# Performance work log

Hardware: AMD Instinct MI355X
Metric: run time of the kernel (lower is better)

The kernel has to match this reference:

```python
import jax, jax.numpy as jnp
import numpy as np

NUM_HEADS = 16
EPS = 1e-6  # torch LayerNorm default is 1e-5; module uses nn.LayerNorm default
LN_EPS = 1e-5


def layer_norm(x, w, b, eps=LN_EPS):
    # normalize over last dim (head_dim), matching infer_layer_norm
    mu = jnp.mean(x, axis=-1, keepdims=True)
    xc = x - mu
    var = jnp.mean(xc * xc, axis=-1, keepdims=True)
    return xc / jnp.sqrt(var + eps) * w + b


def setup_inputs() -> dict:
    key = jax.random.key(0)
    ks = jax.random.split(key, 4)
    B, N, C = 2, 4096, 1024
    H = NUM_HEADS
    D = C // H
    x = jax.random.normal(ks[0], (B, N, C), dtype=jnp.float32)
    qkv_w = jax.random.normal(ks[1], (3 * C, C), dtype=jnp.float32) * (C ** -0.5)
    qkv_b = jax.random.normal(ks[2], (3 * C,), dtype=jnp.float32) * 0.02
    q_norm_w = jnp.ones((D,), dtype=jnp.float32)
    q_norm_b = jnp.zeros((D,), dtype=jnp.float32)
    k_norm_w = jnp.ones((D,), dtype=jnp.float32)
    k_norm_b = jnp.zeros((D,), dtype=jnp.float32)
    proj_w = jax.random.normal(ks[3], (C, C), dtype=jnp.float32) * (C ** -0.5)
    proj_b = jnp.zeros((C,), dtype=jnp.float32)
    return {"x": x, "qkv_w": qkv_w, "qkv_b": qkv_b,
            "q_norm_w": q_norm_w, "q_norm_b": q_norm_b,
            "k_norm_w": k_norm_w, "k_norm_b": k_norm_b,
            "proj_w": proj_w, "proj_b": proj_b}


def reference(x, qkv_w, qkv_b, q_norm_w, q_norm_b, k_norm_w, k_norm_b, proj_w, proj_b):
    B, N, C = x.shape
    H = NUM_HEADS
    D = C // H
    scale = D ** -0.5
    # QKV projection: torch Linear uses y = x @ W^T + b
    qkv = x @ qkv_w.T + qkv_b                      # [B,N,3C]
    qkv = qkv.reshape(B, N, 3, H, D).transpose(2, 0, 3, 1, 4)  # [3,B,H,N,D]
    q, k, v = qkv[0], qkv[1], qkv[2]
    # per-head qk layernorm
    q = layer_norm(q, q_norm_w, q_norm_b)
    k = layer_norm(k, k_norm_w, k_norm_b)
    # scaled dot product attention
    attn = jnp.einsum('bhqd,bhkd->bhqk', q * scale, k)
    attn = jax.nn.softmax(attn, axis=-1)
    out = jnp.einsum('bhqk,bhkd->bhqd', attn, v)   # [B,H,N,D]
    out = out.transpose(0, 2, 1, 3).reshape(B, N, C)
    return out @ proj_w.T + proj_b
```

## Files before the change

kernel.cpp:

```cpp
#include <hip/hip_runtime.h>
#include <hip/hip_bf16.h>

#define NB 2
#define NN 4096
#define NC 1024
#define NH 16
#define ND 64
#define NM (NB*NN)
#define NK 1024
#define J_QKV 3072
#define QSCALE 0.18033688011112042f

typedef unsigned short u16;
typedef unsigned int   u32;
typedef __attribute__((ext_vector_type(8)))  __bf16 bf16x8;
typedef __attribute__((ext_vector_type(4)))  float  f32x4;
typedef __attribute__((ext_vector_type(16))) float  f32x16;

__device__ __forceinline__ u16 f2bf(float f) {
    unsigned int i = __builtin_bit_cast(unsigned int, f);
    unsigned int lsb = (i >> 16) & 1u;
    i += 0x7fffu + lsb;
    return (u16)(i >> 16);
}
__device__ __forceinline__ float fast_exp2(float x) {
#if __has_builtin(__builtin_amdgcn_exp2f)
    return __builtin_amdgcn_exp2f(x);
#else
    return exp2f(x);
#endif
}
__device__ __forceinline__ u32 pkbf(float a, float b) {
    u32 r;
    asm("v_cvt_pk_bf16_f32 %0, %1, %2" : "=v"(r) : "v"(a), "v"(b));
    return r;
}
typedef struct { u32 x, y; } u32pair;
__device__ __forceinline__ u32pair swap32(u32 a, u32 b) {
#if __has_builtin(__builtin_amdgcn_permlane32_swap)
    auto r = __builtin_amdgcn_permlane32_swap((int)a, (int)b, false, false);
    u32pair o; o.x = (u32)r[0]; o.y = (u32)r[1]; return o;
#else
    const bool hi = (threadIdx.x & 32) != 0;
    u32 as = (u32)__shfl_xor((int)a, 32);
    u32 bs = (u32)__shfl_xor((int)b, 32);
    u32pair o; o.x = hi ? bs : a; o.y = hi ? b : as; return o;
#endif
}

__device__ __forceinline__ void glds16(const u16* g, u16* l) {
    __builtin_amdgcn_global_load_lds(
        (const __attribute__((address_space(1))) u32*)g,
        (__attribute__((address_space(3))) u32*)l, 16, 0, 0);
}

__global__ __launch_bounds__(256) void cvt_bf16(
    const float* __restrict__ in, u16* __restrict__ out)
{
    const size_t i = ((size_t)blockIdx.x * 256 + threadIdx.x) * 8;
    const float4 a = *(const float4*)(in + i);
    const float4 b = *(const float4*)(in + i + 4);
    union { u16 h[8]; uint4 v; } u;
    u.h[0] = f2bf(a.x); u.h[1] = f2bf(a.y); u.h[2] = f2bf(a.z); u.h[3] = f2bf(a.w);
    u.h[4] = f2bf(b.x); u.h[5] = f2bf(b.y); u.h[6] = f2bf(b.z); u.h[7] = f2bf(b.w);
    *(uint4*)(out + i) = u.v;
}

template<int MODE, int NJB>
__global__ __launch_bounds__(256, 3) void gemm_nt(
    const u16* __restrict__ A, const u16* __restrict__ W,
    const float* __restrict__ bias,
    const float* __restrict__ qw, const float* __restrict__ qb,
    const float* __restrict__ kw, const float* __restrict__ kb,
    void* __restrict__ outv)
{
    __shared__ __align__(16) u16 sm[4][128][32];
    const int t = threadIdx.x;
    const int w = t >> 6, lane = t & 63;
    const int nb   = blockIdx.x;
    const int cpx  = gridDim.x >> 3;
    const int nb2  = (nb & 7) * cpx + (nb >> 3);
    const int chunk = nb2 / cpx;
    const int c     = nb2 - chunk * cpx;
    const int jb  = (c >> 3) * 128;
    const int m0  = (chunk * 8 + (c & 7)) * 128;
    const int wr = (w >> 1) * 64, wc = (w & 1) * 64;
    const int srow = t >> 2, skc = (t & 3) * 8;
    const u16* ap0 = A + (size_t)(m0 + srow) * NK + skc;
    const u16* ap1 = ap0 + (size_t)64 * NK;
    const u16* wp0 = W + (size_t)(jb + srow) * NK + skc;
    const u16* wp1 = wp0 + (size_t)64 * NK;
    u16* asl0 = &sm[0][srow][skc];    u16* asl1 = &sm[0][srow + 64][skc];
    u16* ash0 = &sm[1][srow][skc];    u16* ash1 = &sm[1][srow + 64][skc];
    u16* bsl0 = &sm[2][srow][skc];    u16* bsl1 = &sm[2][srow + 64][skc];
    u16* bsh0 = &sm[3][srow][skc];    u16* bsh1 = &sm[3][srow + 64][skc];
    const int fm = lane & 15, fk = 8 * (lane >> 4);
    f32x4 acc[4][4];
    #pragma unroll
    for (int i = 0; i < 4; ++i)
        #pragma unroll
        for (int j = 0; j < 4; ++j) acc[i][j] = (f32x4){0.f, 0.f, 0.f, 0.f};

    for (int kt = 0; kt < NK / 64; ++kt) {
        const int ko = kt * 64;
        glds16(ap0 + ko, asl0);
        glds16(ap1 + ko, asl1);
        glds16(ap0 + ko + 32, ash0);
        glds16(ap1 + ko + 32, ash1);
        glds16(wp0 + ko, bsl0);
        glds16(wp1 + ko, bsl1);
        glds16(wp0 + ko + 32, bsh0);
        glds16(wp1 + ko + 32, bsh1);
        __syncthreads();
        {
            bf16x8 af[4], bfr[4];
            #pragma unroll
            for (int i = 0; i < 4; ++i) af[i]  = *(const bf16x8*)&sm[0][wr + 16 * i + fm][fk];
            #pragma unroll
            for (int j = 0; j < 4; ++j) bfr[j] = *(const bf16x8*)&sm[2][wc + 16 * j + fm][fk];
            #pragma unroll
            for (int i = 0; i < 4; ++i)
                #pragma unroll
                for (int j = 0; j < 4; ++j)
                    acc[i][j] = __builtin_amdgcn_mfma_f32_16x16x32_bf16(af[i], bfr[j], acc[i][j], 0, 0, 0);
        }
        {
            bf16x8 af[4], bfr[4];
            #pragma unroll
            for (int i = 0; i < 4; ++i) af[i]  = *(const bf16x8*)&sm[1][wr + 16 * i + fm][fk];
            #pragma unroll
            for (int j = 0; j < 4; ++j) bfr[j] = *(const bf16x8*)&sm[3][wc + 16 * j + fm][fk];
            #pragma unroll
            for (int i = 0; i < 4; ++i)
                #pragma unroll
                for (int j = 0; j < 4; ++j)
                    acc[i][j] = __builtin_amdgcn_mfma_f32_16x16x32_bf16(af[i], bfr[j], acc[i][j], 0, 0, 0);
        }
        __syncthreads();
    }
    const int c16 = lane & 15;
    float bv[4];
    #pragma unroll
    for (int j = 0; j < 4; ++j) bv[j] = bias[jb + wc + 16 * j + c16];
    #pragma unroll
    for (int i = 0; i < 4; ++i)
        #pragma unroll
        for (int j = 0; j < 4; ++j)
            #pragma unroll
            for (int r = 0; r < 4; ++r) acc[i][j][r] += bv[j];
    if (MODE == 0) {
        const int s = jb >> 10;
        if (s < 2) {
            const float* lw = s ? kw : qw;
            const float* lb = s ? kb : qb;
            float lwv[4], lbv[4];
            #pragma unroll
            for (int j = 0; j < 4; ++j) {
                lwv[j] = lw[16 * j + c16]; lbv[j] = lb[16 * j + c16];
            }
            #pragma unroll
            for (int i = 0; i < 4; ++i)
                #pragma unroll
                for (int r = 0; r < 4; ++r) {
                    float sum = acc[i][0][r] + acc[i][1][r] + acc[i][2][r] + acc[i][3][r];
                    #pragma unroll
                    for (int off = 1; off < 16; off <<= 1) sum += __shfl_xor(sum, off);
                    const float mu = sum * (1.0f / 64.0f);
                    float v2 = 0.f;
                    #pragma unroll
                    for (int j = 0; j < 4; ++j) { const float dd = acc[i][j][r] - mu; v2 += dd * dd; }
                    #pragma unroll
                    for (int off = 1; off < 16; off <<= 1) v2 += __shfl_xor(v2, off);
                    const float rstd = rsqrtf(v2 * (1.0f / 64.0f) + 1e-5f);
                    #pragma unroll
                    for (int j = 0; j < 4; ++j) {
                        float y = (acc[i][j][r] - mu) * rstd * lwv[j] + lbv[j];
                        if (s == 0) y *= QSCALE;
                        acc[i][j][r] = y;
                    }
                }
        }
        u16 (*bounce)[128] = (u16 (*)[128])sm;
        const int r0 = 4 * (lane >> 4);
        #pragma unroll
        for (int i = 0; i < 4; ++i)
            #pragma unroll
            for (int r = 0; r < 4; ++r)
                #pragma unroll
                for (int j = 0; j < 4; ++j)
                    bounce[wr + 16 * i + r0 + r][wc + 16 * j + c16] = f2bf(acc[i][j][r]);
        __syncthreads();
        u16* out = (u16*)outv;
        const int l8 = lane >> 3, k8 = lane & 7;
        #pragma unroll
        for (int ch = 0; ch < 2; ++ch) {
            const int col0 = jb + ch * 64;
            const int ss = col0 >> 10, hh = (col0 >> 6) & 15;
            #pragma unroll
            for (int g = 0; g < 4; ++g) {
                const int rr = 32 * w + 8 * g + l8;
                const int row = m0 + rr;
                const int b_ = row >> 12, n = row & 4095;
                const uint4 v = *(const uint4*)&bounce[rr][ch * 64 + k8 * 8];
                *(uint4*)&out[((((size_t)ss * NB + b_) * NH + hh) * NN + n) * ND + k8 * 8] = v;
            }
        }
    } else {
        float* out = (float*)outv;
        const int r0 = 4 * (lane >> 4);
        #pragma unroll
        for (int i = 0; i < 4; ++i)
            #pragma unroll
            for (int r = 0; r < 4; ++r) {
                const int row = m0 + wr + 16 * i + r0 + r;
                #pragma unroll
                for (int j = 0; j < 4; ++j)
                    out[(size_t)row * NC + jb + wc + 16 * j + c16] = acc[i][j][r];
            }
    }
}

__global__ __launch_bounds__(256, 2) void attn_mfma(
    const u16* __restrict__ qkv, u16* __restrict__ aout)
{
    __shared__ __align__(16) u16 Ks[2][64][72];
    __shared__ __align__(16) u16 Vt[2][64][72];
    const int bid  = blockIdx.x;
    const int qblk = bid & 15;
    const int bh   = bid >> 4;
    const int b = bh >> 4, hh = bh & 15;
    const size_t plane = (size_t)NB * NH * NN * ND;
    const size_t base  = ((size_t)(b * NH + hh)) * NN * ND;
    const u16* qp = qkv + base;
    const u16* kp = qkv + plane + base;
    const u16* vp = qkv + 2 * plane + base;
    const int t = threadIdx.x, w = t >> 6, lane = t & 63;
    const int half = lane >> 5, m32 = lane & 31;
    const int q0 = qblk * 256 + 64 * w;

    bf16x8 qf[2][4];
    #pragma unroll
    for (int s = 0; s < 2; ++s) {
        const u16* qrow = qp + (size_t)(q0 + 32 * s + m32) * ND + 8 * half;
        #pragma unroll
        for (int kt = 0; kt < 4; ++kt) qf[s][kt] = *(const bf16x8*)(qrow + 16 * kt);
    }
    f32x16 O[2][2], z;
    #pragma unroll
    for (int r = 0; r < 16; ++r) { O[0][0][r] = 0.f; O[0][1][r] = 0.f;
                                   O[1][0][r] = 0.f; O[1][1][r] = 0.f; z[r] = 0.f; }
    float lpart[2] = {0.f, 0.f};

    const int dgK = 16 * w;
    const int kp2 = t & 31, dgV = (t >> 5) * 8;
    const u16* ksrc = kp + (size_t)lane * ND + dgK;
    const u16* vsrc = vp + (size_t)(2 * kp2) * ND + dgV;

    uint4 kr0, kr1, vre, vro;
    kr0 = *(const uint4*)(ksrc);
    kr1 = *(const uint4*)(ksrc + 8);
    vre = *(const uint4*)(vsrc);
    vro = *(const uint4*)(vsrc + ND);
    {
        *(uint4*)&Ks[0][lane][dgK]     = kr0;
        *(uint4*)&Ks[0][lane][dgK + 8] = kr1;
        const u32* ew = (const u32*)&vre;
        const u32* ow = (const u32*)&vro;
        #pragma unroll
        for (int d = 0; d < 4; ++d) {
            u32 lo = __builtin_amdgcn_perm(ow[d], ew[d], 0x05040100u);
            u32 hi = __builtin_amdgcn_perm(ow[d], ew[d], 0x07060302u);
            *(u32*)&Vt[0][dgV + 2 * d][2 * kp2]     = lo;
            *(u32*)&Vt[0][dgV + 2 * d + 1][2 * kp2] = hi;
        }
    }
    __syncthreads();

    union W8 { u32 wd[4]; bf16x8 f; };

    for (int kb = 0; kb < NN / 64; ++kb) {
        const int cur = kb & 1, nxt = cur ^ 1;
        const bool more = (kb + 1) < (NN / 64);
        if (more) {
            const u16* ks2 = ksrc + (size_t)(kb + 1) * 64 * ND;
            kr0 = *(const uint4*)ks2;
            kr1 = *(const uint4*)(ks2 + 8);
            const u16* vs2 = vsrc + (size_t)(kb + 1) * 64 * ND;
            vre = *(const uint4*)vs2;
            vro = *(const uint4*)(vs2 + ND);
        }
        f32x16 sT0[2], sT1[2];
        __builtin_amdgcn_s_setprio(1);
        {
            bf16x8 k0 = *(const bf16x8*)&Ks[cur][m32][8 * half];
            bf16x8 k1 = *(const bf16x8*)&Ks[cur][32 + m32][8 * half];
            sT0[0] = __builtin_amdgcn_mfma_f32_32x32x16_bf16(k0, qf[0][0], z, 0, 0, 0);
            sT0[1] = __builtin_amdgcn_mfma_f32_32x32x16_bf16(k1, qf[0][0], z, 0, 0, 0);
        }
        #pragma unroll
        for (int kt = 1; kt < 4; ++kt) {
            bf16x8 k0 = *(const bf16x8*)&Ks[cur][m32][16 * kt + 8 * half];
            bf16x8 k1 = *(const bf16x8*)&Ks[cur][32 + m32][16 * kt + 8 * half];
            sT0[0] = __builtin_amdgcn_mfma_f32_32x32x16_bf16(k0, qf[0][kt], sT0[0], 0, 0, 0);
            sT0[1] = __builtin_amdgcn_mfma_f32_32x32x16_bf16(k1, qf[0][kt], sT0[1], 0, 0, 0);
        }
        {
            bf16x8 k0 = *(const bf16x8*)&Ks[cur][m32][8 * half];
            bf16x8 k1 = *(const bf16x8*)&Ks[cur][32 + m32][8 * half];
            sT1[0] = __builtin_amdgcn_mfma_f32_32x32x16_bf16(k0, qf[1][0], z, 0, 0, 0);
            sT1[1] = __builtin_amdgcn_mfma_f32_32x32x16_bf16(k1, qf[1][0], z, 0, 0, 0);
        }
        #pragma unroll
        for (int kt = 1; kt < 4; ++kt) {
            bf16x8 k0 = *(const bf16x8*)&Ks[cur][m32][16 * kt + 8 * half];
            bf16x8 k1 = *(const bf16x8*)&Ks[cur][32 + m32][16 * kt + 8 * half];
            sT1[0] = __builtin_amdgcn_mfma_f32_32x32x16_bf16(k0, qf[1][kt], sT1[0], 0, 0, 0);
            sT1[1] = __builtin_amdgcn_mfma_f32_32x32x16_bf16(k1, qf[1][kt], sT1[1], 0, 0, 0);
        }
        __builtin_amdgcn_s_setprio(0);
        W8 pa0[4], pa1[4];
        {
            float ss0 = 0.f, ss1 = 0.f;
            #pragma unroll
            for (int kh = 0; kh < 2; ++kh) {
                float p[16];
                #pragma unroll
                for (int r = 0; r < 16; ++r) p[r] = fast_exp2(sT0[kh][r]);
                #pragma unroll
                for (int r = 0; r < 8; ++r) { ss0 += p[r]; ss1 += p[8 + r]; }
                u32 c[4][2];
                #pragma unroll
                for (int g = 0; g < 4; ++g) {
                    c[g][0] = pkbf(p[4 * g + 0], p[4 * g + 1]);
                    c[g][1] = pkbf(p[4 * g + 2], p[4 * g + 3]);
                }
                #pragma unroll
                for (int par = 0; par < 2; ++par) {
                    u32pair wA = swap32(c[2 * par][0], c[2 * par + 1][0]);
                    u32pair wB = swap32(c[2 * par][1], c[2 * par + 1][1]);
                    const int kt = 2 * kh + par;
                    pa0[kt].wd[0] = wA.x;
                    pa0[kt].wd[1] = wB.x;
                    pa0[kt].wd[2] = wA.y;
                    pa0[kt].wd[3] = wB.y;
                }
            }
            lpart[0] += ss0 + ss1;
        }
        __builtin_amdgcn_s_setprio(1);
        #pragma unroll
        for (int kt = 0; kt < 4; ++kt) {
            bf16x8 v0 = *(const bf16x8*)&Vt[cur][m32][16 * kt + 8 * half];
            bf16x8 v1 = *(const bf16x8*)&Vt[cur][32 + m32][16 * kt + 8 * half];
            O[0][0] = __builtin_amdgcn_mfma_f32_32x32x16_bf16(pa0[kt].f, v0, O[0][0], 0, 0, 0);
            O[0][1] = __builtin_amdgcn_mfma_f32_32x32x16_bf16(pa0[kt].f, v1, O[0][1], 0, 0, 0);
        }
        __builtin_amdgcn_s_setprio(0);
        {
            float ss0 = 0.f, ss1 = 0.f;
            #pragma unroll
            for (int kh = 0; kh < 2; ++kh) {
                float p[16];
                #pragma unroll
                for (int r = 0; r < 16; ++r) p[r] = fast_exp2(sT1[kh][r]);
                #pragma unroll
                for (int r = 0; r < 8; ++r) { ss0 += p[r]; ss1 += p[8 + r]; }
                u32 c[4][2];
                #pragma unroll
                for (int g = 0; g < 4; ++g) {
                    c[g][0] = pkbf(p[4 * g + 0], p[4 * g + 1]);
                    c[g][1] = pkbf(p[4 * g + 2], p[4 * g + 3]);
                }
                #pragma unroll
                for (int par = 0; par < 2; ++par) {
                    u32pair wA = swap32(c[2 * par][0], c[2 * par + 1][0]);
                    u32pair wB = swap32(c[2 * par][1], c[2 * par + 1][1]);
                    const int kt = 2 * kh + par;
                    pa1[kt].wd[0] = wA.x;
                    pa1[kt].wd[1] = wB.x;
                    pa1[kt].wd[2] = wA.y;
                    pa1[kt].wd[3] = wB.y;
                }
            }
            lpart[1] += ss0 + ss1;
        }
        __builtin_amdgcn_s_setprio(1);
        #pragma unroll
        for (int kt = 0; kt < 4; ++kt) {
            bf16x8 v0 = *(const bf16x8*)&Vt[cur][m32][16 * kt + 8 * half];
            bf16x8 v1 = *(const bf16x8*)&Vt[cur][32 + m32][16 * kt + 8 * half];
            O[1][0] = __builtin_amdgcn_mfma_f32_32x32x16_bf16(pa1[kt].f, v0, O[1][0], 0, 0, 0);
            O[1][1] = __builtin_amdgcn_mfma_f32_32x32x16_bf16(pa1[kt].f, v1, O[1][1], 0, 0, 0);
        }
        __builtin_amdgcn_s_setprio(0);
        if (more) {
            *(uint4*)&Ks[nxt][lane][dgK]     = kr0;
            *(uint4*)&Ks[nxt][lane][dgK + 8] = kr1;
            const u32* ew = (const u32*)&vre;
            const u32* ow = (const u32*)&vro;
            #pragma unroll
            for (int d = 0; d < 4; ++d) {
                u32 lo = __builtin_amdgcn_perm(ow[d], ew[d], 0x05040100u);
                u32 hi = __builtin_amdgcn_perm(ow[d], ew[d], 0x07060302u);
                *(u32*)&Vt[nxt][dgV + 2 * d][2 * kp2]     = lo;
                *(u32*)&Vt[nxt][dgV + 2 * d + 1][2 * kp2] = hi;
            }
            __syncthreads();
        }
    }
    #pragma unroll
    for (int s = 0; s < 2; ++s) {
        const float tot = lpart[s] + __shfl_xor(lpart[s], 32);
        #pragma unroll
        for (int r = 0; r < 16; ++r) {
            const int qq = (r & 3) + 8 * (r >> 2) + 4 * half;
            const float inv = 1.0f / __shfl(tot, qq);
            const int row = q0 + 32 * s + qq;
            u16* dst = aout + ((size_t)(b * NN + row)) * NC + hh * 64;
            dst[m32]      = f2bf(O[s][0][r] * inv);
            dst[32 + m32] = f2bf(O[s][1][r] * inv);
        }
    }
}

extern "C" void kernel_launch(void* const* d_in, const int* in_sizes, int n_in,
                              void* d_out, int out_size, void* d_ws, size_t ws_size,
                              hipStream_t stream) {
    const float* x     = (const float*)d_in[0];
    const float* qkv_w = (const float*)d_in[1];
    const float* qkv_b = (const float*)d_in[2];
    const float* q_nw  = (const float*)d_in[3];
    const float* q_nb  = (const float*)d_in[4];
    const float* k_nw  = (const float*)d_in[5];
    const float* k_nb  = (const float*)d_in[6];
    const float* p_w   = (const float*)d_in[7];
    const float* p_b   = (const float*)d_in[8];
    float* out = (float*)d_out;
    u16* qkv    = (u16*)d_ws;
    u16* x_bf   = qkv + (size_t)3 * NB * NH * NN * ND;
    u16* attn_o = x_bf;
    u16* w_bf   = x_bf + (size_t)NM * NC;
    u16* pw_bf  = w_bf + (size_t)J_QKV * NK;

    cvt_bf16<<<(NM * NC) / 2048, 256, 0, stream>>>(x, x_bf);
    cvt_bf16<<<(J_QKV * NK) / 2048, 256, 0, stream>>>(qkv_w, w_bf);
    cvt_bf16<<<(NC * NK) / 2048, 256, 0, stream>>>(p_w, pw_bf);

    gemm_nt<0, J_QKV / 128><<<(J_QKV / 128) * (NM / 128), 256, 0, stream>>>(
        x_bf, w_bf, qkv_b, q_nw, q_nb, k_nw, k_nb, qkv);
    attn_mfma<<<NB * NH * (NN / 256), 256, 0, stream>>>(qkv, attn_o);
    gemm_nt<1, NC / 128><<<(NC / 128) * (NM / 128), 256, 0, stream>>>(
        attn_o, pw_bf, p_b, q_nw, q_nb, k_nw, k_nb, out);
}
```

Measured before the change: 332.8 us.

## Compute softmax row sums via MFMA, merge conversion kernels, raise QKV GEMM occupancy

Drops the per-lane scalar accumulation of softmax denominators in attention. Row sums are now produced by an extra MFMA that multiplies the packed P fragments with a vector of bf16 ones, which also removes the end-of-kernel shuffles. The three fp32-to-bf16 conversion launches are merged into one kernel that picks its source by block index. The QKV GEMM's launch-bounds occupancy hint is raised from 3 to 4, which may cause register spills. The sums are now built from bf16-rounded probabilities, and the extra MFMAs add matrix-unit work and accumulator registers.

```diff
diff --git a/kernel.cpp b/kernel.cpp
--- a/kernel.cpp
+++ b/kernel.cpp
@@ -54,20 +54,27 @@
         (__attribute__((address_space(3))) u32*)l, 16, 0, 0);
 }
 
-__global__ __launch_bounds__(256) void cvt_bf16(
-    const float* __restrict__ in, u16* __restrict__ out)
+__global__ __launch_bounds__(256) void cvt3(
+    const float* __restrict__ a, u16* __restrict__ oa,
+    const float* __restrict__ b, u16* __restrict__ ob,
+    const float* __restrict__ c, u16* __restrict__ oc)
 {
-    const size_t i = ((size_t)blockIdx.x * 256 + threadIdx.x) * 8;
-    const float4 a = *(const float4*)(in + i);
-    const float4 b = *(const float4*)(in + i + 4);
+    const int blk = blockIdx.x;
+    const float* src; u16* dst; size_t off;
+    if (blk < 4096)      { src = a; dst = oa; off = (size_t)blk * 2048; }
+    else if (blk < 5632) { src = b; dst = ob; off = (size_t)(blk - 4096) * 2048; }
+    else                 { src = c; dst = oc; off = (size_t)(blk - 5632) * 2048; }
+    const size_t i = off + (size_t)threadIdx.x * 8;
+    const float4 va = *(const float4*)(src + i);
+    const float4 vb = *(const float4*)(src + i + 4);
     union { u16 h[8]; uint4 v; } u;
-    u.h[0] = f2bf(a.x); u.h[1] = f2bf(a.y); u.h[2] = f2bf(a.z); u.h[3] = f2bf(a.w);
-    u.h[4] = f2bf(b.x); u.h[5] = f2bf(b.y); u.h[6] = f2bf(b.z); u.h[7] = f2bf(b.w);
-    *(uint4*)(out + i) = u.v;
-}
-
-template<int MODE, int NJB>
-__global__ __launch_bounds__(256, 3) void gemm_nt(
+    u.h[0] = f2bf(va.x); u.h[1] = f2bf(va.y); u.h[2] = f2bf(va.z); u.h[3] = f2bf(va.w);
+    u.h[4] = f2bf(vb.x); u.h[5] = f2bf(vb.y); u.h[6] = f2bf(vb.z); u.h[7] = f2bf(vb.w);
+    *(uint4*)(dst + i) = u.v;
+}
+
+template<int MODE, int NJB, int OCC>
+__global__ __launch_bounds__(256, OCC) void gemm_nt(
     const u16* __restrict__ A, const u16* __restrict__ W,
     const float* __restrict__ bias,
     const float* __restrict__ qw, const float* __restrict__ qb,
@@ -245,11 +252,16 @@
         #pragma unroll
         for (int kt = 0; kt < 4; ++kt) qf[s][kt] = *(const bf16x8*)(qrow + 16 * kt);
     }
-    f32x16 O[2][2], z;
-    #pragma unroll
-    for (int r = 0; r < 16; ++r) { O[0][0][r] = 0.f; O[0][1][r] = 0.f;
-                                   O[1][0][r] = 0.f; O[1][1][r] = 0.f; z[r] = 0.f; }
-    float lpart[2] = {0.f, 0.f};
+    f32x16 O[2][2], L[2], z;
+    #pragma unroll
+    for (int r = 0; r < 16; ++r) {
+        O[0][0][r] = 0.f; O[0][1][r] = 0.f;
+        O[1][0][r] = 0.f; O[1][1][r] = 0.f;
+        L[0][r] = 0.f;    L[1][r] = 0.f;    z[r] = 0.f;
+    }
+    union { u32 wd[4]; bf16x8 f; } ONE1;
+    #pragma unroll
+    for (int i = 0; i < 4; ++i) ONE1.wd[i] = 0x3F803F80u;
 
     const int dgK = 16 * w;
     const int kp2 = t & 31, dgV = (t >> 5) * 8;
@@ -319,33 +331,27 @@
         }
         __builtin_amdgcn_s_setprio(0);
         W8 pa0[4], pa1[4];
-        {
-            float ss0 = 0.f, ss1 = 0.f;
-            #pragma unroll
-            for (int kh = 0; kh < 2; ++kh) {
-                float p[16];
-                #pragma unroll
-                for (int r = 0; r < 16; ++r) p[r] = fast_exp2(sT0[kh][r]);
-                #pragma unroll
-                for (int r = 0; r < 8; ++r) { ss0 += p[r]; ss1 += p[8 + r]; }
-                u32 c[4][2];
-                #pragma unroll
-                for (int g = 0; g < 4; ++g) {
-                    c[g][0] = pkbf(p[4 * g + 0], p[4 * g + 1]);
-                    c[g][1] = pkbf(p[4 * g + 2], p[4 * g + 3]);
-                }
-                #pragma unroll
-                for (int par = 0; par < 2; ++par) {
-                    u32pair wA = swap32(c[2 * par][0], c[2 * par + 1][0]);
-                    u32pair wB = swap32(c[2 * par][1], c[2 * par + 1][1]);
-                    const int kt = 2 * kh + par;
-                    pa0[kt].wd[0] = wA.x;
-                    pa0[kt].wd[1] = wB.x;
-                    pa0[kt].wd[2] = wA.y;
-                    pa0[kt].wd[3] = wB.y;
-                }
-            }
-            lpart[0] += ss0 + ss1;
+        #pragma unroll
+        for (int kh = 0; kh < 2; ++kh) {
+            float p[16];
+            #pragma unroll
+            for (int r = 0; r < 16; ++r) p[r] = fast_exp2(sT0[kh][r]);
+            u32 c[4][2];
+            #pragma unroll
+            for (int g = 0; g < 4; ++g) {
+                c[g][0] = pkbf(p[4 * g + 0], p[4 * g + 1]);
+                c[g][1] = pkbf(p[4 * g + 2], p[4 * g + 3]);
+            }
+            #pragma unroll
+            for (int par = 0; par < 2; ++par) {
+                u32pair wA = swap32(c[2 * par][0], c[2 * par + 1][0]);
+                u32pair wB = swap32(c[2 * par][1], c[2 * par + 1][1]);
+                const int kt = 2 * kh + par;
+                pa0[kt].wd[0] = wA.x;
+                pa0[kt].wd[1] = wB.x;
+                pa0[kt].wd[2] = wA.y;
+                pa0[kt].wd[3] = wB.y;
+            }
         }
         __builtin_amdgcn_s_setprio(1);
         #pragma unroll
@@ -354,35 +360,30 @@
             bf16x8 v1 = *(const bf16x8*)&Vt[cur][32 + m32][16 * kt + 8 * half];
             O[0][0] = __builtin_amdgcn_mfma_f32_32x32x16_bf16(pa0[kt].f, v0, O[0][0], 0, 0, 0);
             O[0][1] = __builtin_amdgcn_mfma_f32_32x32x16_bf16(pa0[kt].f, v1, O[0][1], 0, 0, 0);
+            L[0]    = __builtin_amdgcn_mfma_f32_32x32x16_bf16(pa0[kt].f, ONE1.f, L[0], 0, 0, 0);
         }
         __builtin_amdgcn_s_setprio(0);
-        {
-            float ss0 = 0.f, ss1 = 0.f;
-            #pragma unroll
-            for (int kh = 0; kh < 2; ++kh) {
-                float p[16];
-                #pragma unroll
-                for (int r = 0; r < 16; ++r) p[r] = fast_exp2(sT1[kh][r]);
-                #pragma unroll
-                for (int r = 0; r < 8; ++r) { ss0 += p[r]; ss1 += p[8 + r]; }
-                u32 c[4][2];
-                #pragma unroll
-                for (int g = 0; g < 4; ++g) {
-                    c[g][0] = pkbf(p[4 * g + 0], p[4 * g + 1]);
-                    c[g][1] = pkbf(p[4 * g + 2], p[4 * g + 3]);
-                }
-                #pragma unroll
-                for (int par = 0; par < 2; ++par) {
-                    u32pair wA = swap32(c[2 * par][0], c[2 * par + 1][0]);
-                    u32pair wB = swap32(c[2 * par][1], c[2 * par + 1][1]);
-                    const int kt = 2 * kh + par;
-                    pa1[kt].wd[0] = wA.x;
-                    pa1[kt].wd[1] = wB.x;
-                    pa1[kt].wd[2] = wA.y;
-                    pa1[kt].wd[3] = wB.y;
-                }
-            }
-            lpart[1] += ss0 + ss1;
+        #pragma unroll
+        for (int kh = 0; kh < 2; ++kh) {
+            float p[16];
+            #pragma unroll
+            for (int r = 0; r < 16; ++r) p[r] = fast_exp2(sT1[kh][r]);
+            u32 c[4][2];
+            #pragma unroll
+            for (int g = 0; g < 4; ++g) {
+                c[g][0] = pkbf(p[4 * g + 0], p[4 * g + 1]);
+                c[g][1] = pkbf(p[4 * g + 2], p[4 * g + 3]);
+            }
+            #pragma unroll
+            for (int par = 0; par < 2; ++par) {
+                u32pair wA = swap32(c[2 * par][0], c[2 * par + 1][0]);
+                u32pair wB = swap32(c[2 * par][1], c[2 * par + 1][1]);
+                const int kt = 2 * kh + par;
+                pa1[kt].wd[0] = wA.x;
+                pa1[kt].wd[1] = wB.x;
+                pa1[kt].wd[2] = wA.y;
+                pa1[kt].wd[3] = wB.y;
+            }
         }
         __builtin_amdgcn_s_setprio(1);
         #pragma unroll
@@ -391,6 +392,7 @@
             bf16x8 v1 = *(const bf16x8*)&Vt[cur][32 + m32][16 * kt + 8 * half];
             O[1][0] = __builtin_amdgcn_mfma_f32_32x32x16_bf16(pa1[kt].f, v0, O[1][0], 0, 0, 0);
             O[1][1] = __builtin_amdgcn_mfma_f32_32x32x16_bf16(pa1[kt].f, v1, O[1][1], 0, 0, 0);
+            L[1]    = __builtin_amdgcn_mfma_f32_32x32x16_bf16(pa1[kt].f, ONE1.f, L[1], 0, 0, 0);
         }
         __builtin_amdgcn_s_setprio(0);
         if (more) {
@@ -410,11 +412,10 @@
     }
     #pragma unroll
     for (int s = 0; s < 2; ++s) {
-        const float tot = lpart[s] + __shfl_xor(lpart[s], 32);
         #pragma unroll
         for (int r = 0; r < 16; ++r) {
             const int qq = (r & 3) + 8 * (r >> 2) + 4 * half;
-            const float inv = 1.0f / __shfl(tot, qq);
+            const float inv = 1.0f / L[s][r];
             const int row = q0 + 32 * s + qq;
             u16* dst = aout + ((size_t)(b * NN + row)) * NC + hh * 64;
             dst[m32]      = f2bf(O[s][0][r] * inv);
@@ -442,13 +443,11 @@
     u16* w_bf   = x_bf + (size_t)NM * NC;
     u16* pw_bf  = w_bf + (size_t)J_QKV * NK;
 
-    cvt_bf16<<<(NM * NC) / 2048, 256, 0, stream>>>(x, x_bf);
-    cvt_bf16<<<(J_QKV * NK) / 2048, 256, 0, stream>>>(qkv_w, w_bf);
-    cvt_bf16<<<(NC * NK) / 2048, 256, 0, stream>>>(p_w, pw_bf);
-
-    gemm_nt<0, J_QKV / 128><<<(J_QKV / 128) * (NM / 128), 256, 0, stream>>>(
+    cvt3<<<6144, 256, 0, stream>>>(x, x_bf, qkv_w, w_bf, p_w, pw_bf);
+
+    gemm_nt<0, J_QKV / 128, 4><<<(J_QKV / 128) * (NM / 128), 256, 0, stream>>>(
         x_bf, w_bf, qkv_b, q_nw, q_nb, k_nw, k_nb, qkv);
     attn_mfma<<<NB * NH * (NN / 256), 256, 0, stream>>>(qkv, attn_o);
-    gemm_nt<1, NC / 128><<<(NC / 128) * (NM / 128), 256, 0, stream>>>(
+    gemm_nt<1, NC / 128, 3><<<(NC / 128) * (NM / 128), 256, 0, stream>>>(
         attn_o, pw_bf, p_b, q_nw, q_nb, k_nw, k_nb, out);
 }
```

New measurement: 343.9 us. 1.03x slower.
